# Kernel tuning notes

Hardware: AMD Instinct MI355X
Metric: run time of the kernel (lower is better)

The kernel has to match this reference:

```python
import jax, jax.numpy as jnp
import numpy as np

# dims
B, S, E, H, W = 32, 256, 512, 512, 512   # batch, max_sentence_length, word_emb, rnn_units, weight_size
ENC = 2 * H                               # bidirectional encoder hidden
V = 50000                                 # vocab


def setup_inputs() -> dict:
    key = jax.random.key(0)
    ks = jax.random.split(key, 16)
    n = jax.random.normal
    return {
        "word_ids": jax.random.randint(ks[0], (B, S), 0, V),
        "encoder_outputs": n(ks[1], (B, S, ENC), jnp.float32),
        "encoder_hn": n(ks[2], (B, H), jnp.float32),          # initial decoder cell state
        "emb": n(ks[3], (V, E), jnp.float32) * 0.02,          # WordFeature embedding table
        "chunk_emb": n(ks[4], (S, W), jnp.float32) * 0.02,    # chunk_length_embedding
        "W1": n(ks[5], (ENC, W), jnp.float32) / np.sqrt(ENC),
        "W2": n(ks[6], (E, W), jnp.float32) / np.sqrt(E),
        "W3": n(ks[7], (E, W), jnp.float32) / np.sqrt(E),
        "W4": n(ks[8], (H, W), jnp.float32) / np.sqrt(H),
        "vt1": n(ks[9], (W,), jnp.float32) / np.sqrt(W),
        "vt2": n(ks[10], (W,), jnp.float32) / np.sqrt(W),
        "Wx": n(ks[11], (E, 4 * H), jnp.float32) / np.sqrt(E),  # decoder LSTM cell
        "Wh": n(ks[12], (H, 4 * H), jnp.float32) / np.sqrt(H),
        "bias": jnp.zeros((4 * H,), jnp.float32),
    }


def reference(word_ids, encoder_outputs, encoder_hn, emb, chunk_emb,
              W1, W2, W3, W4, vt1, vt2, Wx, Wh, bias):
    Ss = word_ids.shape[1]
    Hh = encoder_hn.shape[1]
    inp = emb[word_ids]                                   # [B,S,E] word features
    b1 = jnp.einsum('bse,ew->bsw', encoder_outputs, W1)   # W1(encoder_output), hoisted
    b2 = jnp.einsum('bse,ew->bsw', inp, W2)               # W2(single_input), hoisted
    pos = jnp.arange(Ss)

    def decode_one(inp_b, b1_b, b2_b, c0):
        def step(carry, _):
            last_bond, bond, h, c, out_vec = carry
            done = bond >= Ss
            # decoder input: mean of current segment inp[last_bond:bond] (zeros at step 0)
            m = ((pos >= last_bond) & (pos < bond)).astype(inp_b.dtype)  # [S]
            x = (m @ inp_b) / jnp.maximum(m.sum(), 1.0)                  # [E]
            # LSTM cell (stand-in for decoder.pointer_forward)
            gates = x @ Wx + h @ Wh + bias                               # [4H]
            i_g, f_g, g_g, o_g = jnp.split(gates, 4)
            c_n = jax.nn.sigmoid(f_g) * c + jax.nn.sigmoid(i_g) * jnp.tanh(g_g)
            h_n = jax.nn.sigmoid(o_g) * jnp.tanh(c_n)
            h2 = jnp.where(done, h, h_n)
            c2 = jnp.where(done, c, c_n)
            bidx = jnp.minimum(bond, Ss - 1)
            # pointer attention over positions >= bond
            blend = jnp.tanh(b1_b + b2_b + inp_b[bidx] @ W3 + h2 @ W4)   # [S,W]
            seg_len = jnp.clip(bond - last_bond, 0, Ss - 1)
            scores = blend @ vt1 + chunk_emb[seg_len] @ vt2              # [S]
            scores = jnp.where(pos >= bidx, scores, -1e30)
            # log_softmax is monotonic -> argmax of scores == argmax of log-probs
            idx = jnp.argmax(scores)                                     # absolute = max_index + bond
            new_bond = jnp.where(idx > bond, idx, bond + 1)              # force progress
            widx = jnp.minimum(new_bond, Ss - 1)
            val = jnp.where((~done) & (new_bond < Ss), 1.0, out_vec[widx])
            out_new = out_vec.at[widx].set(val)
            last2 = jnp.where(done, last_bond, bond)
            bond2 = jnp.where(done, bond, new_bond)
            return (last2, bond2, h2, c2, out_new), None

        init = (jnp.int32(0), jnp.int32(0),
                jnp.zeros((Hh,), inp_b.dtype), c0,
                jnp.zeros((Ss,), inp_b.dtype))
        (_, _, _, _, out_vec), _ = jax.lax.scan(step, init, None, length=Ss)
        return out_vec

    outs = jax.vmap(decode_one)(inp, b1, b2, encoder_hn)   # [B,S]
    return outs.T                                          # [S,B] == torch.stack(output_list, 1)
```

## Files before the change

### kernel.cpp

```cpp
#include <hip/hip_runtime.h>
#include <math.h>

#define Bn   32
#define Sn   256
#define En   512
#define Hn   512
#define Wn   512
#define ENCn 1024
#define G4   2048
#define KTOT 1536

#define OFF_BSUM  0L
#define OFF_U3    4194304L
#define OFF_PE    8388608L
#define OFF_WXB   12599296L
#define OFF_WHB   13647872L
#define OFF_W4B   14696448L
#define OFF_GXW   14958592L
#define OFF_GPH   15089664L
#define OFF_SPART 15220736L
#define OFF_STATE 15482880L

typedef unsigned long long u64t;

__device__ __forceinline__ float aload(const float* p) {
    return __hip_atomic_load(p, __ATOMIC_RELAXED, __HIP_MEMORY_SCOPE_AGENT);
}
__device__ __forceinline__ void astore(float* p, float v) {
    __hip_atomic_store(p, v, __ATOMIC_RELAXED, __HIP_MEMORY_SCOPE_AGENT);
}
__device__ __forceinline__ int aiload(const int* p) {
    return __hip_atomic_load(p, __ATOMIC_RELAXED, __HIP_MEMORY_SCOPE_AGENT);
}
__device__ __forceinline__ void aistore(int* p, int v) {
    __hip_atomic_store(p, v, __ATOMIC_RELAXED, __HIP_MEMORY_SCOPE_AGENT);
}
__device__ __forceinline__ u64t aload64(const u64t* p) {
    return __hip_atomic_load(p, __ATOMIC_RELAXED, __HIP_MEMORY_SCOPE_AGENT);
}
__device__ __forceinline__ void astore64(u64t* p, u64t v) {
    __hip_atomic_store(p, v, __ATOMIC_RELAXED, __HIP_MEMORY_SCOPE_AGENT);
}
__device__ __forceinline__ u64t pack2(float a, float b) {
    return (u64t)__float_as_uint(a) | ((u64t)__float_as_uint(b) << 32);
}
__device__ __forceinline__ u64t packtag(float a, int t) {
    return (u64t)__float_as_uint(a) | ((u64t)(unsigned)t << 32);
}
__device__ __forceinline__ float lo32(u64t v) { return __uint_as_float((unsigned)(v & 0xffffffffu)); }
__device__ __forceinline__ float hi32(u64t v) { return __uint_as_float((unsigned)(v >> 32)); }

__global__ void init_kernel(float* __restrict__ gxw, float* __restrict__ gph,
                            float* __restrict__ sp2, int* __restrict__ state)
{
    int i = blockIdx.x * blockDim.x + threadIdx.x;
    if (i < 131072) { gxw[i] = 0.0f; gph[i] = 0.0f; }
    if (i < 262144) sp2[i] = 0.0f;
    if (i < 8192) state[i] = (i < 512) ? 1 : 0;
}

__global__ void wtrans_kernel(const float* __restrict__ Wx, const float* __restrict__ Wh,
                              const float* __restrict__ W4, float* __restrict__ WxB,
                              float* __restrict__ WhB, float* __restrict__ W4B)
{
    int idx = blockIdx.x * 256 + threadIdx.x;
    if (idx < 1048576) {
        const int c = idx & 255, k = (idx >> 8) & 511, cb = idx >> 17;
        WxB[idx] = Wx[(long)k * G4 + cb * 256 + c];
        WhB[idx] = Wh[(long)k * G4 + cb * 256 + c];
    }
    if (idx < 262144) {
        const int cc = idx & 3, l = (idx >> 2) & 63, kq = (idx >> 8) & 127, cb = idx >> 15;
        const int k = 4 * kq + cc, j = cb * 64 + l;
        W4B[idx] = W4[(long)k * Wn + j];
    }
}

__global__ void pe1_kernel(const int* __restrict__ wid, const float* __restrict__ emb,
                           float* __restrict__ pb)
{
    const int b = blockIdx.x, blk = blockIdx.y;
    __shared__ int wids[16];
    if (threadIdx.x < 16) wids[threadIdx.x] = wid[b * Sn + blk * 16 + threadIdx.x];
    __syncthreads();
    float a0 = 0.f, a1 = 0.f;
    for (int s = 0; s < 16; ++s) {
        const float* r = emb + (long)wids[s] * En;
        a0 += r[threadIdx.x]; a1 += r[threadIdx.x + 256];
    }
    pb[((long)b * 16 + blk) * En + threadIdx.x] = a0;
    pb[((long)b * 16 + blk) * En + threadIdx.x + 256] = a1;
}

__global__ void pe2_kernel(const int* __restrict__ wid, const float* __restrict__ emb,
                           const float* __restrict__ pb, float* __restrict__ pe)
{
    const int b = blockIdx.x, blk = blockIdx.y;
    __shared__ int wids[16];
    if (threadIdx.x < 16) wids[threadIdx.x] = wid[b * Sn + blk * 16 + threadIdx.x];
    __syncthreads();
    float a0 = 0.f, a1 = 0.f;
    for (int j = 0; j < blk; ++j) {
        a0 += pb[((long)b * 16 + j) * En + threadIdx.x];
        a1 += pb[((long)b * 16 + j) * En + threadIdx.x + 256];
    }
    float* base = pe + (long)b * 257 * En;
    if (blk == 0) { base[threadIdx.x] = 0.f; base[threadIdx.x + 256] = 0.f; }
    for (int s = 0; s < 16; ++s) {
        const float* r = emb + (long)wids[s] * En;
        a0 += r[threadIdx.x]; a1 += r[threadIdx.x + 256];
        float* o = base + (long)(blk * 16 + s + 1) * En;
        o[threadIdx.x] = a0; o[threadIdx.x + 256] = a1;
    }
}

__global__ __launch_bounds__(256) void bsum_gemm(
    const float* __restrict__ enc, const int* __restrict__ wid,
    const float* __restrict__ emb, const float* __restrict__ W1,
    const float* __restrict__ W2, float* __restrict__ bsum)
{
    __shared__ float As[16][68];
    __shared__ float Bs[16][68];
    const int tid  = threadIdx.x;
    const int row0 = blockIdx.y * 64;
    const int col0 = blockIdx.x * 64;
    const int tm0  = (tid & 15) * 4;
    const int tn0  = (tid >> 4) * 4;
    const int la_r = tid >> 2;
    const int la_k = (tid & 3) * 4;
    const int lb_k = tid >> 4;
    const int lb_n = (tid & 15) * 4;

    float acc[4][4];
#pragma unroll
    for (int i = 0; i < 4; i++)
#pragma unroll
        for (int j = 0; j < 4; j++) acc[i][j] = 0.0f;

    for (int k0 = 0; k0 < KTOT; k0 += 16) {
        const int gr = row0 + la_r;
        float4 av;
        if (k0 < ENCn) {
            av = *(const float4*)&enc[(long)gr * ENCn + k0 + la_k];
        } else {
            const int wv = wid[gr];
            av = *(const float4*)&emb[(long)wv * En + (k0 - ENCn) + la_k];
        }
        As[la_k + 0][la_r] = av.x;
        As[la_k + 1][la_r] = av.y;
        As[la_k + 2][la_r] = av.z;
        As[la_k + 3][la_r] = av.w;
        float4 bv;
        if (k0 < ENCn) bv = *(const float4*)&W1[(long)(k0 + lb_k) * Wn + col0 + lb_n];
        else           bv = *(const float4*)&W2[(long)(k0 - ENCn + lb_k) * Wn + col0 + lb_n];
        *(float4*)&Bs[lb_k][lb_n] = bv;
        __syncthreads();
#pragma unroll
        for (int kk = 0; kk < 16; kk++) {
            float4 a = *(const float4*)&As[kk][tm0];
            float4 b = *(const float4*)&Bs[kk][tn0];
            acc[0][0] += a.x * b.x; acc[0][1] += a.x * b.y; acc[0][2] += a.x * b.z; acc[0][3] += a.x * b.w;
            acc[1][0] += a.y * b.x; acc[1][1] += a.y * b.y; acc[1][2] += a.y * b.z; acc[1][3] += a.y * b.w;
            acc[2][0] += a.z * b.x; acc[2][1] += a.z * b.y; acc[2][2] += a.z * b.z; acc[2][3] += a.z * b.w;
            acc[3][0] += a.w * b.x; acc[3][1] += a.w * b.y; acc[3][2] += a.w * b.z; acc[3][3] += a.w * b.w;
        }
        __syncthreads();
    }
#pragma unroll
    for (int i = 0; i < 4; i++) {
        float4 o = make_float4(acc[i][0], acc[i][1], acc[i][2], acc[i][3]);
        *(float4*)&bsum[(long)(row0 + tm0 + i) * Wn + col0 + tn0] = o;
    }
}

__global__ __launch_bounds__(256) void u3_gemm(
    const int* __restrict__ wid, const float* __restrict__ emb,
    const float* __restrict__ W3, float* __restrict__ u3)
{
    __shared__ float As[16][68];
    __shared__ float Bs[16][68];
    const int tid  = threadIdx.x;
    const int row0 = blockIdx.y * 64;
    const int col0 = blockIdx.x * 64;
    const int tm0  = (tid & 15) * 4;
    const int tn0  = (tid >> 4) * 4;
    const int la_r = tid >> 2;
    const int la_k = (tid & 3) * 4;
    const int lb_k = tid >> 4;
    const int lb_n = (tid & 15) * 4;

    float acc[4][4];
#pragma unroll
    for (int i = 0; i < 4; i++)
#pragma unroll
        for (int j = 0; j < 4; j++) acc[i][j] = 0.0f;

    for (int k0 = 0; k0 < 512; k0 += 16) {
        const int gr = row0 + la_r;
        const int wv = wid[gr];
        float4 av = *(const float4*)&emb[(long)wv * En + k0 + la_k];
        As[la_k + 0][la_r] = av.x;
        As[la_k + 1][la_r] = av.y;
        As[la_k + 2][la_r] = av.z;
        As[la_k + 3][la_r] = av.w;
        *(float4*)&Bs[lb_k][lb_n] = *(const float4*)&W3[(long)(k0 + lb_k) * Wn + col0 + lb_n];
        __syncthreads();
#pragma unroll
        for (int kk = 0; kk < 16; kk++) {
            float4 a = *(const float4*)&As[kk][tm0];
            float4 b = *(const float4*)&Bs[kk][tn0];
            acc[0][0] += a.x * b.x; acc[0][1] += a.x * b.y; acc[0][2] += a.x * b.z; acc[0][3] += a.x * b.w;
            acc[1][0] += a.y * b.x; acc[1][1] += a.y * b.y; acc[1][2] += a.y * b.z; acc[1][3] += a.y * b.w;
            acc[2][0] += a.z * b.x; acc[2][1] += a.z * b.y; acc[2][2] += a.z * b.z; acc[2][3] += a.z * b.w;
            acc[3][0] += a.w * b.x; acc[3][1] += a.w * b.y; acc[3][2] += a.w * b.z; acc[3][3] += a.w * b.w;
        }
        __syncthreads();
    }
#pragma unroll
    for (int i = 0; i < 4; i++) {
        float4 o = make_float4(acc[i][0], acc[i][1], acc[i][2], acc[i][3]);
        *(float4*)&u3[(long)(row0 + tm0 + i) * Wn + col0 + tn0] = o;
    }
}

__global__ __launch_bounds__(256) void decode_kernel(
    const float* __restrict__ bias, const float* __restrict__ vt1,
    const float* __restrict__ bsum, const float* __restrict__ u3,
    const float* __restrict__ pe,   const float* __restrict__ WxB,
    const float* __restrict__ WhB,  const float* __restrict__ W4B,
    float* __restrict__ gxwbuf, float* __restrict__ gphbuf,
    u64t* __restrict__ spart2, int* __restrict__ state,
    const float* __restrict__ hn0, float* __restrict__ out)
{
    __shared__ __align__(16) float wlds[32768];
    __shared__ __align__(16) float hld[512];
    __shared__ __align__(16) float cld[512];
    __shared__ __align__(16) float xld[512];
    __shared__ __align__(16) float sgp[4][256];
    __shared__ __align__(16) float sred4[4][64];
    __shared__ float qv[64];
    __shared__ float s_svt[64];
    __shared__ float s_wv[4];
    __shared__ int   s_wi[4];

    const int wg   = blockIdx.x;
    const int tid  = threadIdx.x;
    const int lane = tid & 63;
    const int wv   = tid >> 6;
    const int b    = wg >> 3;
    const int cb2  = wg & 7;

    int* gflag = state;
    u64t* gxw64 = (u64t*)gxwbuf;
    u64t* gph64 = (u64t*)gphbuf;
    const float4* W4B4 = (const float4*)W4B;
    float4* wlds4 = (float4*)wlds;
    const float4* h4 = (const float4*)hld;
    const float2* pef2 = (const float2*)pe;

    {
        const float4* src = W4B4 + (long)cb2 * 8192;
        for (int i = tid; i < 8192; i += 256) wlds4[i] = src[i];
    }
    if (tid < 64) s_svt[tid] = vt1[cb2 * 64 + tid];
    cld[tid]       = hn0[b * Hn + tid];
    cld[256 + tid] = hn0[b * Hn + 256 + tid];
    hld[tid] = 0.f; hld[256 + tid] = 0.f;
    const float2* bias2 = (const float2*)bias;
    const float2 bi  = bias2[tid];
    const float2 bf  = bias2[256 + tid];
    const float2 bg_ = bias2[512 + tid];
    const float2 bo  = bias2[768 + tid];
    __syncthreads();

    int bd = 0, ls = 0;

    for (int t = 1; t <= Sn; ++t) {
        const long cur = (long)(t & 1) * 32768;
        const long scur = (long)(t & 1) * 65536;

        if (tid < 8) {
            const int* g = gflag + 16 * b + tid;
            while (aiload(g) < t) __builtin_amdgcn_s_sleep(1);
        }
        __syncthreads();
        float u3v = 0.f;
        if (tid < 64) u3v = aload(&u3[((long)b * Sn + bd) * Wn + cb2 * 64 + tid]);
        const long gb = cur + (long)b * 1024;
        const u64t gx0 = aload64(&gxw64[gb + tid]);
        const u64t gx1 = aload64(&gxw64[gb + 256 + tid]);
        const u64t gx2 = aload64(&gxw64[gb + 512 + tid]);
        const u64t gx3 = aload64(&gxw64[gb + 768 + tid]);
        const u64t gh0 = aload64(&gph64[gb + tid]);
        const u64t gh1 = aload64(&gph64[gb + 256 + tid]);
        const u64t gh2 = aload64(&gph64[gb + 512 + tid]);
        const u64t gh3 = aload64(&gph64[gb + 768 + tid]);

        {
            const int j0 = 2 * tid, j1 = j0 + 1;
            const float igA = lo32(gx0) + lo32(gh0) + bi.x;
            const float igB = hi32(gx0) + hi32(gh0) + bi.y;
            const float fgA = lo32(gx1) + lo32(gh1) + bf.x;
            const float fgB = hi32(gx1) + hi32(gh1) + bf.y;
            const float ggA = lo32(gx2) + lo32(gh2) + bg_.x;
            const float ggB = hi32(gx2) + hi32(gh2) + bg_.y;
            const float ogA = lo32(gx3) + lo32(gh3) + bo.x;
            const float ogB = hi32(gx3) + hi32(gh3) + bo.y;
            const float sfA = 1.f / (1.f + expf(-fgA));
            const float siA = 1.f / (1.f + expf(-igA));
            const float soA = 1.f / (1.f + expf(-ogA));
            const float cnA = sfA * cld[j0] + siA * tanhf(ggA);
            const float h2A = soA * tanhf(cnA);
            const float sfB = 1.f / (1.f + expf(-fgB));
            const float siB = 1.f / (1.f + expf(-igB));
            const float soB = 1.f / (1.f + expf(-ogB));
            const float cnB = sfB * cld[j1] + siB * tanhf(ggB);
            const float h2B = soB * tanhf(cnB);
            cld[j0] = cnA; hld[j0] = h2A;
            cld[j1] = cnB; hld[j1] = h2B;
        }
        __syncthreads();

        {
            float acc = 0.f;
            const float4* wr = wlds4 + (wv * 32) * 64 + lane;
#pragma unroll 8
            for (int kq = 0; kq < 32; ++kq) {
                const float4 w = wr[kq * 64];
                const float4 hv = h4[wv * 32 + kq];
                acc += w.x * hv.x + w.y * hv.y + w.z * hv.z + w.w * hv.w;
            }
            sred4[wv][lane] = acc;
        }
        __syncthreads();
        if (tid < 64) qv[tid] = sred4[0][tid] + sred4[1][tid] + sred4[2][tid] + sred4[3][tid] + u3v;
        __syncthreads();

        if (tid >= bd) {
            const float* row = bsum + ((long)b * Sn + tid) * Wn + cb2 * 64;
            float a = 0.f;
#pragma unroll 8
            for (int i = 0; i < 64; ++i)
                a += tanhf(row[i] + qv[i]) * s_svt[i];
            astore64(&spart2[scur + (long)b * 2048 + cb2 * 256 + tid], packtag(a, t));
        }

        float v = -3.402823e38f; int vi = Sn;
        if (tid >= bd) {
            const u64t* sp = spart2 + scur + (long)b * 2048 + tid;
            u64t e0, e1, e2, e3, e4, e5, e6, e7;
            for (;;) {
                e0 = aload64(&sp[0]);    e1 = aload64(&sp[256]);
                e2 = aload64(&sp[512]);  e3 = aload64(&sp[768]);
                e4 = aload64(&sp[1024]); e5 = aload64(&sp[1280]);
                e6 = aload64(&sp[1536]); e7 = aload64(&sp[1792]);
                const unsigned tt = (unsigned)t;
                if ((unsigned)(e0 >> 32) == tt && (unsigned)(e1 >> 32) == tt &&
                    (unsigned)(e2 >> 32) == tt && (unsigned)(e3 >> 32) == tt &&
                    (unsigned)(e4 >> 32) == tt && (unsigned)(e5 >> 32) == tt &&
                    (unsigned)(e6 >> 32) == tt && (unsigned)(e7 >> 32) == tt) break;
                __builtin_amdgcn_s_sleep(1);
            }
            v = lo32(e0) + lo32(e1) + lo32(e2) + lo32(e3)
              + lo32(e4) + lo32(e5) + lo32(e6) + lo32(e7);
            vi = tid;
        }
#pragma unroll
        for (int off = 32; off; off >>= 1) {
            const float v2 = __shfl_xor(v, off, 64);
            const int   i2 = __shfl_xor(vi, off, 64);
            if (v2 > v || (v2 == v && i2 < vi)) { v = v2; vi = i2; }
        }
        if (lane == 0) { s_wv[wv] = v; s_wi[wv] = vi; }
        __syncthreads();
        {
            float bv = s_wv[0]; int bi_ = s_wi[0];
#pragma unroll
            for (int k = 1; k < 4; ++k)
                if (s_wv[k] > bv || (s_wv[k] == bv && s_wi[k] < bi_)) { bv = s_wv[k]; bi_ = s_wi[k]; }
            const int nb = (bi_ > bd) ? bi_ : bd + 1;
            if (cb2 == 0 && tid == 0 && nb < Sn) out[nb * Bn + b] = 1.0f;
            ls = bd; bd = nb;
        }
        __syncthreads();
        if (bd >= Sn) break;

        const long nxt = (long)((t + 1) & 1) * 32768;
        const float2 pa  = pef2[((long)b * 257 + bd) * 256 + tid];
        const float2 pb_ = pef2[((long)b * 257 + ls) * 256 + tid];
        {
            float4 acc = make_float4(0.f, 0.f, 0.f, 0.f);
            const float* wb = WhB + (long)cb2 * 131072;
            const int k0 = wv * 128;
#pragma unroll 4
            for (int k = k0; k < k0 + 128; ++k) {
                const float hk = hld[k];
                const float4 w = *(const float4*)&wb[(long)k * 256 + lane * 4];
                acc.x += hk * w.x; acc.y += hk * w.y; acc.z += hk * w.z; acc.w += hk * w.w;
            }
            *(float4*)&sgp[wv][lane * 4] = acc;
        }
        {
            const float inv = 1.0f / (float)max(bd - ls, 1);
            xld[2 * tid]     = (pa.x - pb_.x) * inv;
            xld[2 * tid + 1] = (pa.y - pb_.y) * inv;
        }
        __syncthreads();
        if (tid < 128) {
            const int c0 = 2 * tid, c1 = c0 + 1;
            const float lo = sgp[0][c0] + sgp[1][c0] + sgp[2][c0] + sgp[3][c0];
            const float hi = sgp[0][c1] + sgp[1][c1] + sgp[2][c1] + sgp[3][c1];
            astore64(&gph64[nxt + (long)b * 1024 + cb2 * 128 + tid], pack2(lo, hi));
        }
        __syncthreads();
        {
            float4 acc = make_float4(0.f, 0.f, 0.f, 0.f);
            const float* wb = WxB + (long)cb2 * 131072;
            const int k0 = wv * 128;
#pragma unroll 4
            for (int k = k0; k < k0 + 128; ++k) {
                const float xk = xld[k];
                const float4 w = *(const float4*)&wb[(long)k * 256 + lane * 4];
                acc.x += xk * w.x; acc.y += xk * w.y; acc.z += xk * w.z; acc.w += xk * w.w;
            }
            *(float4*)&sgp[wv][lane * 4] = acc;
        }
        __syncthreads();
        if (tid < 128) {
            const int c0 = 2 * tid, c1 = c0 + 1;
            const float lo = sgp[0][c0] + sgp[1][c0] + sgp[2][c0] + sgp[3][c0];
            const float hi = sgp[0][c1] + sgp[1][c1] + sgp[2][c1] + sgp[3][c1];
            astore64(&gxw64[nxt + (long)b * 1024 + cb2 * 128 + tid], pack2(lo, hi));
        }
        __syncthreads();
        if (tid == 0) aistore(&gflag[16 * b + cb2], t + 1);
    }
}

extern "C" void kernel_launch(void* const* d_in, const int* in_sizes, int n_in,
                              void* d_out, int out_size, void* d_ws, size_t ws_size,
                              hipStream_t stream)
{
    const int*   wid  = (const int*)d_in[0];
    const float* enc  = (const float*)d_in[1];
    const float* hn0  = (const float*)d_in[2];
    const float* emb  = (const float*)d_in[3];
    const float* W1   = (const float*)d_in[5];
    const float* W2   = (const float*)d_in[6];
    const float* W3   = (const float*)d_in[7];
    const float* W4   = (const float*)d_in[8];
    const float* vt1  = (const float*)d_in[9];
    const float* Wx   = (const float*)d_in[11];
    const float* Wh   = (const float*)d_in[12];
    const float* bias = (const float*)d_in[13];

    float* ws    = (float*)d_ws;
    float* bsum  = ws + OFF_BSUM;
    float* u3    = ws + OFF_U3;
    float* pe    = ws + OFF_PE;
    float* WxB   = ws + OFF_WXB;
    float* WhB   = ws + OFF_WHB;
    float* W4B   = ws + OFF_W4B;
    float* gxw   = ws + OFF_GXW;
    float* gph   = ws + OFF_GPH;
    float* sp2f  = ws + OFF_SPART;
    u64t*  sp2   = (u64t*)sp2f;
    int*   state = (int*)(ws + OFF_STATE);
    float* out   = (float*)d_out;
    float* pb    = ws + OFF_BSUM;

    (void)hipMemsetAsync(d_out, 0, (size_t)Sn * Bn * sizeof(float), stream);
    hipLaunchKernelGGL(init_kernel, dim3(1024), dim3(256), 0, stream, gxw, gph, sp2f, state);
    hipLaunchKernelGGL(wtrans_kernel, dim3(4096), dim3(256), 0, stream, Wx, Wh, W4, WxB, WhB, W4B);
    hipLaunchKernelGGL(pe1_kernel, dim3(32, 16), dim3(256), 0, stream, wid, emb, pb);
    hipLaunchKernelGGL(pe2_kernel, dim3(32, 16), dim3(256), 0, stream, wid, emb, pb, pe);
    hipLaunchKernelGGL(u3_gemm, dim3(8, 128), dim3(256), 0, stream, wid, emb, W3, u3);
    hipLaunchKernelGGL(bsum_gemm, dim3(8, 128), dim3(256), 0, stream, enc, wid, emb, W1, W2, bsum);

    void* args[] = { (void*)&bias, (void*)&vt1, (void*)&bsum, (void*)&u3, (void*)&pe,
                     (void*)&WxB, (void*)&WhB, (void*)&W4B, (void*)&gxw, (void*)&gph,
                     (void*)&sp2, (void*)&state, (void*)&hn0, (void*)&out };
    (void)hipLaunchCooperativeKernel((void*)decode_kernel, dim3(256), dim3(256), args, 0, stream);
}
```

Before: 787.4 us.

## Replace per-step flag barrier with tagged gate values and hoist Wh matvec

After: 809.4 us. 2.8% more time.

```diff
diff --git a/kernel.cpp b/kernel.cpp
--- a/kernel.cpp
+++ b/kernel.cpp
@@ -17,46 +17,37 @@
 #define OFF_WHB   13647872L
 #define OFF_W4B   14696448L
 #define OFF_GXW   14958592L
-#define OFF_GPH   15089664L
-#define OFF_SPART 15220736L
-#define OFF_STATE 15482880L
+#define OFF_GPH   15220736L
+#define OFF_SPART 15482880L
+#define OFF_STATE 15745024L
 
 typedef unsigned long long u64t;
 
 __device__ __forceinline__ float aload(const float* p) {
     return __hip_atomic_load(p, __ATOMIC_RELAXED, __HIP_MEMORY_SCOPE_AGENT);
 }
-__device__ __forceinline__ void astore(float* p, float v) {
-    __hip_atomic_store(p, v, __ATOMIC_RELAXED, __HIP_MEMORY_SCOPE_AGENT);
-}
-__device__ __forceinline__ int aiload(const int* p) {
-    return __hip_atomic_load(p, __ATOMIC_RELAXED, __HIP_MEMORY_SCOPE_AGENT);
-}
-__device__ __forceinline__ void aistore(int* p, int v) {
-    __hip_atomic_store(p, v, __ATOMIC_RELAXED, __HIP_MEMORY_SCOPE_AGENT);
-}
 __device__ __forceinline__ u64t aload64(const u64t* p) {
     return __hip_atomic_load(p, __ATOMIC_RELAXED, __HIP_MEMORY_SCOPE_AGENT);
 }
 __device__ __forceinline__ void astore64(u64t* p, u64t v) {
     __hip_atomic_store(p, v, __ATOMIC_RELAXED, __HIP_MEMORY_SCOPE_AGENT);
 }
-__device__ __forceinline__ u64t pack2(float a, float b) {
-    return (u64t)__float_as_uint(a) | ((u64t)__float_as_uint(b) << 32);
-}
 __device__ __forceinline__ u64t packtag(float a, int t) {
     return (u64t)__float_as_uint(a) | ((u64t)(unsigned)t << 32);
 }
 __device__ __forceinline__ float lo32(u64t v) { return __uint_as_float((unsigned)(v & 0xffffffffu)); }
-__device__ __forceinline__ float hi32(u64t v) { return __uint_as_float((unsigned)(v >> 32)); }
-
-__global__ void init_kernel(float* __restrict__ gxw, float* __restrict__ gph,
-                            float* __restrict__ sp2, int* __restrict__ state)
+
+__global__ void init_kernel(u64t* __restrict__ gxw64, u64t* __restrict__ gph64,
+                            u64t* __restrict__ sp64, int* __restrict__ state)
 {
     int i = blockIdx.x * blockDim.x + threadIdx.x;
-    if (i < 131072) { gxw[i] = 0.0f; gph[i] = 0.0f; }
-    if (i < 262144) sp2[i] = 0.0f;
-    if (i < 8192) state[i] = (i < 512) ? 1 : 0;
+    if (i < 131072) {
+        const u64t gv = (i < 65536) ? 0ULL : packtag(0.0f, 1);
+        gxw64[i] = gv;
+        gph64[i] = gv;
+        sp64[i]  = 0ULL;
+    }
+    if (i < 8192) state[i] = 0;
 }
 
 __global__ void wtrans_kernel(const float* __restrict__ Wx, const float* __restrict__ Wh,
@@ -228,8 +219,8 @@
     const float* __restrict__ bsum, const float* __restrict__ u3,
     const float* __restrict__ pe,   const float* __restrict__ WxB,
     const float* __restrict__ WhB,  const float* __restrict__ W4B,
-    float* __restrict__ gxwbuf, float* __restrict__ gphbuf,
-    u64t* __restrict__ spart2, int* __restrict__ state,
+    u64t* __restrict__ gxw64, u64t* __restrict__ gph64,
+    u64t* __restrict__ spart2,
     const float* __restrict__ hn0, float* __restrict__ out)
 {
     __shared__ __align__(16) float wlds[32768];
@@ -250,9 +241,6 @@
     const int b    = wg >> 3;
     const int cb2  = wg & 7;
 
-    int* gflag = state;
-    u64t* gxw64 = (u64t*)gxwbuf;
-    u64t* gph64 = (u64t*)gphbuf;
     const float4* W4B4 = (const float4*)W4B;
     float4* wlds4 = (float4*)wlds;
     const float4* h4 = (const float4*)hld;
@@ -276,36 +264,50 @@
     int bd = 0, ls = 0;
 
     for (int t = 1; t <= Sn; ++t) {
-        const long cur = (long)(t & 1) * 32768;
+        const long cur  = (long)(t & 1) * 65536;
         const long scur = (long)(t & 1) * 65536;
 
-        if (tid < 8) {
-            const int* g = gflag + 16 * b + tid;
-            while (aiload(g) < t) __builtin_amdgcn_s_sleep(1);
-        }
-        __syncthreads();
         float u3v = 0.f;
         if (tid < 64) u3v = aload(&u3[((long)b * Sn + bd) * Wn + cb2 * 64 + tid]);
-        const long gb = cur + (long)b * 1024;
-        const u64t gx0 = aload64(&gxw64[gb + tid]);
-        const u64t gx1 = aload64(&gxw64[gb + 256 + tid]);
-        const u64t gx2 = aload64(&gxw64[gb + 512 + tid]);
-        const u64t gx3 = aload64(&gxw64[gb + 768 + tid]);
-        const u64t gh0 = aload64(&gph64[gb + tid]);
-        const u64t gh1 = aload64(&gph64[gb + 256 + tid]);
-        const u64t gh2 = aload64(&gph64[gb + 512 + tid]);
-        const u64t gh3 = aload64(&gph64[gb + 768 + tid]);
-
-        {
-            const int j0 = 2 * tid, j1 = j0 + 1;
+
+        const u64t* gxp = gxw64 + cur + (long)b * 2048;
+        const u64t* ghp = gph64 + cur + (long)b * 2048;
+        const int j0 = 2 * tid, j1 = j0 + 1;
+        u64t gx0, gx1, gx2, gx3, gx4, gx5, gx6, gx7;
+        u64t gh0, gh1, gh2, gh3, gh4, gh5, gh6, gh7;
+        {
+            const unsigned tt = (unsigned)t;
+            for (;;) {
+                gx0 = aload64(&gxp[j0]);        gx1 = aload64(&gxp[j1]);
+                gx2 = aload64(&gxp[512 + j0]);  gx3 = aload64(&gxp[512 + j1]);
+                gx4 = aload64(&gxp[1024 + j0]); gx5 = aload64(&gxp[1024 + j1]);
+                gx6 = aload64(&gxp[1536 + j0]); gx7 = aload64(&gxp[1536 + j1]);
+                gh0 = aload64(&ghp[j0]);        gh1 = aload64(&ghp[j1]);
+                gh2 = aload64(&ghp[512 + j0]);  gh3 = aload64(&ghp[512 + j1]);
+                gh4 = aload64(&ghp[1024 + j0]); gh5 = aload64(&ghp[1024 + j1]);
+                gh6 = aload64(&ghp[1536 + j0]); gh7 = aload64(&ghp[1536 + j1]);
+                bool ok = ((unsigned)(gx0 >> 32) == tt) & ((unsigned)(gx1 >> 32) == tt)
+                        & ((unsigned)(gx2 >> 32) == tt) & ((unsigned)(gx3 >> 32) == tt)
+                        & ((unsigned)(gx4 >> 32) == tt) & ((unsigned)(gx5 >> 32) == tt)
+                        & ((unsigned)(gx6 >> 32) == tt) & ((unsigned)(gx7 >> 32) == tt)
+                        & ((unsigned)(gh0 >> 32) == tt) & ((unsigned)(gh1 >> 32) == tt)
+                        & ((unsigned)(gh2 >> 32) == tt) & ((unsigned)(gh3 >> 32) == tt)
+                        & ((unsigned)(gh4 >> 32) == tt) & ((unsigned)(gh5 >> 32) == tt)
+                        & ((unsigned)(gh6 >> 32) == tt) & ((unsigned)(gh7 >> 32) == tt);
+                if (ok) break;
+                __builtin_amdgcn_s_sleep(1);
+            }
+        }
+
+        {
             const float igA = lo32(gx0) + lo32(gh0) + bi.x;
-            const float igB = hi32(gx0) + hi32(gh0) + bi.y;
-            const float fgA = lo32(gx1) + lo32(gh1) + bf.x;
-            const float fgB = hi32(gx1) + hi32(gh1) + bf.y;
-            const float ggA = lo32(gx2) + lo32(gh2) + bg_.x;
-            const float ggB = hi32(gx2) + hi32(gh2) + bg_.y;
-            const float ogA = lo32(gx3) + lo32(gh3) + bo.x;
-            const float ogB = hi32(gx3) + hi32(gh3) + bo.y;
+            const float igB = lo32(gx1) + lo32(gh1) + bi.y;
+            const float fgA = lo32(gx2) + lo32(gh2) + bf.x;
+            const float fgB = lo32(gx3) + lo32(gh3) + bf.y;
+            const float ggA = lo32(gx4) + lo32(gh4) + bg_.x;
+            const float ggB = lo32(gx5) + lo32(gh5) + bg_.y;
+            const float ogA = lo32(gx6) + lo32(gh6) + bo.x;
+            const float ogB = lo32(gx7) + lo32(gh7) + bo.y;
             const float sfA = 1.f / (1.f + expf(-fgA));
             const float siA = 1.f / (1.f + expf(-igA));
             const float soA = 1.f / (1.f + expf(-ogA));
@@ -345,49 +347,6 @@
             astore64(&spart2[scur + (long)b * 2048 + cb2 * 256 + tid], packtag(a, t));
         }
 
-        float v = -3.402823e38f; int vi = Sn;
-        if (tid >= bd) {
-            const u64t* sp = spart2 + scur + (long)b * 2048 + tid;
-            u64t e0, e1, e2, e3, e4, e5, e6, e7;
-            for (;;) {
-                e0 = aload64(&sp[0]);    e1 = aload64(&sp[256]);
-                e2 = aload64(&sp[512]);  e3 = aload64(&sp[768]);
-                e4 = aload64(&sp[1024]); e5 = aload64(&sp[1280]);
-                e6 = aload64(&sp[1536]); e7 = aload64(&sp[1792]);
-                const unsigned tt = (unsigned)t;
-                if ((unsigned)(e0 >> 32) == tt && (unsigned)(e1 >> 32) == tt &&
-                    (unsigned)(e2 >> 32) == tt && (unsigned)(e3 >> 32) == tt &&
-                    (unsigned)(e4 >> 32) == tt && (unsigned)(e5 >> 32) == tt &&
-                    (unsigned)(e6 >> 32) == tt && (unsigned)(e7 >> 32) == tt) break;
-                __builtin_amdgcn_s_sleep(1);
-            }
-            v = lo32(e0) + lo32(e1) + lo32(e2) + lo32(e3)
-              + lo32(e4) + lo32(e5) + lo32(e6) + lo32(e7);
-            vi = tid;
-        }
-#pragma unroll
-        for (int off = 32; off; off >>= 1) {
-            const float v2 = __shfl_xor(v, off, 64);
-            const int   i2 = __shfl_xor(vi, off, 64);
-            if (v2 > v || (v2 == v && i2 < vi)) { v = v2; vi = i2; }
-        }
-        if (lane == 0) { s_wv[wv] = v; s_wi[wv] = vi; }
-        __syncthreads();
-        {
-            float bv = s_wv[0]; int bi_ = s_wi[0];
-#pragma unroll
-            for (int k = 1; k < 4; ++k)
-                if (s_wv[k] > bv || (s_wv[k] == bv && s_wi[k] < bi_)) { bv = s_wv[k]; bi_ = s_wi[k]; }
-            const int nb = (bi_ > bd) ? bi_ : bd + 1;
-            if (cb2 == 0 && tid == 0 && nb < Sn) out[nb * Bn + b] = 1.0f;
-            ls = bd; bd = nb;
-        }
-        __syncthreads();
-        if (bd >= Sn) break;
-
-        const long nxt = (long)((t + 1) & 1) * 32768;
-        const float2 pa  = pef2[((long)b * 257 + bd) * 256 + tid];
-        const float2 pb_ = pef2[((long)b * 257 + ls) * 256 + tid];
         {
             float4 acc = make_float4(0.f, 0.f, 0.f, 0.f);
             const float* wb = WhB + (long)cb2 * 131072;
@@ -400,17 +359,59 @@
             }
             *(float4*)&sgp[wv][lane * 4] = acc;
         }
-        {
+        __syncthreads();
+        {
+            const long nxt = (long)((t + 1) & 1) * 65536;
+            const float val = sgp[0][tid] + sgp[1][tid] + sgp[2][tid] + sgp[3][tid];
+            astore64(&gph64[nxt + (long)b * 2048 + cb2 * 256 + tid], packtag(val, t + 1));
+        }
+
+        float v = -3.402823e38f; int vi = Sn;
+        if (tid >= bd) {
+            const u64t* sp = spart2 + scur + (long)b * 2048 + tid;
+            u64t e0, e1, e2, e3, e4, e5, e6, e7;
+            const unsigned tt = (unsigned)t;
+            for (;;) {
+                e0 = aload64(&sp[0]);    e1 = aload64(&sp[256]);
+                e2 = aload64(&sp[512]);  e3 = aload64(&sp[768]);
+                e4 = aload64(&sp[1024]); e5 = aload64(&sp[1280]);
+                e6 = aload64(&sp[1536]); e7 = aload64(&sp[1792]);
+                if ((unsigned)(e0 >> 32) == tt && (unsigned)(e1 >> 32) == tt &&
+                    (unsigned)(e2 >> 32) == tt && (unsigned)(e3 >> 32) == tt &&
+                    (unsigned)(e4 >> 32) == tt && (unsigned)(e5 >> 32) == tt &&
+                    (unsigned)(e6 >> 32) == tt && (unsigned)(e7 >> 32) == tt) break;
+                __builtin_amdgcn_s_sleep(1);
+            }
+            v = lo32(e0) + lo32(e1) + lo32(e2) + lo32(e3)
+              + lo32(e4) + lo32(e5) + lo32(e6) + lo32(e7);
+            vi = tid;
+        }
+#pragma unroll
+        for (int off = 32; off; off >>= 1) {
+            const float v2 = __shfl_xor(v, off, 64);
+            const int   i2 = __shfl_xor(vi, off, 64);
+            if (v2 > v || (v2 == v && i2 < vi)) { v = v2; vi = i2; }
+        }
+        if (lane == 0) { s_wv[wv] = v; s_wi[wv] = vi; }
+        __syncthreads();
+        {
+            float bv = s_wv[0]; int bi_ = s_wi[0];
+#pragma unroll
+            for (int k = 1; k < 4; ++k)
+                if (s_wv[k] > bv || (s_wv[k] == bv && s_wi[k] < bi_)) { bv = s_wv[k]; bi_ = s_wi[k]; }
+            const int nb = (bi_ > bd) ? bi_ : bd + 1;
+            if (cb2 == 0 && tid == 0 && nb < Sn) out[nb * Bn + b] = 1.0f;
+            ls = bd; bd = nb;
+        }
+        __syncthreads();
+        if (bd >= Sn) break;
+
+        {
+            const float2 pa  = pef2[((long)b * 257 + bd) * 256 + tid];
+            const float2 pb_ = pef2[((long)b * 257 + ls) * 256 + tid];
             const float inv = 1.0f / (float)max(bd - ls, 1);
             xld[2 * tid]     = (pa.x - pb_.x) * inv;
             xld[2 * tid + 1] = (pa.y - pb_.y) * inv;
-        }
-        __syncthreads();
-        if (tid < 128) {
-            const int c0 = 2 * tid, c1 = c0 + 1;
-            const float lo = sgp[0][c0] + sgp[1][c0] + sgp[2][c0] + sgp[3][c0];
-            const float hi = sgp[0][c1] + sgp[1][c1] + sgp[2][c1] + sgp[3][c1];
-            astore64(&gph64[nxt + (long)b * 1024 + cb2 * 128 + tid], pack2(lo, hi));
         }
         __syncthreads();
         {
@@ -426,14 +427,12 @@
             *(float4*)&sgp[wv][lane * 4] = acc;
         }
         __syncthreads();
-        if (tid < 128) {
-            const int c0 = 2 * tid, c1 = c0 + 1;
-            const float lo = sgp[0][c0] + sgp[1][c0] + sgp[2][c0] + sgp[3][c0];
-            const float hi = sgp[0][c1] + sgp[1][c1] + sgp[2][c1] + sgp[3][c1];
-            astore64(&gxw64[nxt + (long)b * 1024 + cb2 * 128 + tid], pack2(lo, hi));
-        }
-        __syncthreads();
-        if (tid == 0) aistore(&gflag[16 * b + cb2], t + 1);
+        {
+            const long nxt = (long)((t + 1) & 1) * 65536;
+            const float val = sgp[0][tid] + sgp[1][tid] + sgp[2][tid] + sgp[3][tid];
+            astore64(&gxw64[nxt + (long)b * 2048 + cb2 * 256 + tid], packtag(val, t + 1));
+        }
+        __syncthreads();
     }
 }
 
@@ -461,16 +460,15 @@
     float* WxB   = ws + OFF_WXB;
     float* WhB   = ws + OFF_WHB;
     float* W4B   = ws + OFF_W4B;
-    float* gxw   = ws + OFF_GXW;
-    float* gph   = ws + OFF_GPH;
-    float* sp2f  = ws + OFF_SPART;
-    u64t*  sp2   = (u64t*)sp2f;
+    u64t*  gxw64 = (u64t*)(ws + OFF_GXW);
+    u64t*  gph64 = (u64t*)(ws + OFF_GPH);
+    u64t*  sp2   = (u64t*)(ws + OFF_SPART);
     int*   state = (int*)(ws + OFF_STATE);
     float* out   = (float*)d_out;
     float* pb    = ws + OFF_BSUM;
 
     (void)hipMemsetAsync(d_out, 0, (size_t)Sn * Bn * sizeof(float), stream);
-    hipLaunchKernelGGL(init_kernel, dim3(1024), dim3(256), 0, stream, gxw, gph, sp2f, state);
+    hipLaunchKernelGGL(init_kernel, dim3(512), dim3(256), 0, stream, gxw64, gph64, sp2, state);
     hipLaunchKernelGGL(wtrans_kernel, dim3(4096), dim3(256), 0, stream, Wx, Wh, W4, WxB, WhB, W4B);
     hipLaunchKernelGGL(pe1_kernel, dim3(32, 16), dim3(256), 0, stream, wid, emb, pb);
     hipLaunchKernelGGL(pe2_kernel, dim3(32, 16), dim3(256), 0, stream, wid, emb, pb, pe);
@@ -478,7 +476,7 @@
     hipLaunchKernelGGL(bsum_gemm, dim3(8, 128), dim3(256), 0, stream, enc, wid, emb, W1, W2, bsum);
 
     void* args[] = { (void*)&bias, (void*)&vt1, (void*)&bsum, (void*)&u3, (void*)&pe,
-                     (void*)&WxB, (void*)&WhB, (void*)&W4B, (void*)&gxw, (void*)&gph,
-                     (void*)&sp2, (void*)&state, (void*)&hn0, (void*)&out };
+                     (void*)&WxB, (void*)&WhB, (void*)&W4B, (void*)&gxw64, (void*)&gph64,
+                     (void*)&sp2, (void*)&hn0, (void*)&out };
     (void)hipLaunchCooperativeKernel((void*)decode_kernel, dim3(256), dim3(256), args, 0, stream);
 }
```
